# Performance work log

Measured on AMD Instinct MI355X. Metric: run time of the kernel, lower is better.

## Reference

```python
import jax, jax.numpy as jnp
from jax import lax
import numpy as np

Bn, DM, HH, WW = 2, 192, 64, 64   # batch, d_model, H, W (H==W required by transpose-stack)
DI = 384   # d_inner = ssm_ratio * d_model
DS = 16    # ssm_d_state
ND = 4     # n_directions
CG = 12    # c_group
LN_EPS = 1e-5


def setup_inputs() -> dict:
    key = jax.random.key(0)
    k = jax.random.split(key, 16)
    w = lambda i, shape: jax.random.normal(k[i], shape, jnp.float32) * 0.05
    return {
        "x": jax.random.normal(k[0], (Bn, DM, HH, WW), jnp.float32),
        "in_proj_w": w(1, (DI, DM)),
        "dwconv_w": w(2, (DI, 1, 3, 3)),
        "dwconv_b": w(3, (DI,)),
        "x_down_w": w(4, (DS, DI)),
        "w_up_w": w(5, (CG * DI, DS)),
        "l_up_w": w(6, (ND * DI, DS)),
        "u_up_w": w(7, (ND * DI, DS)),
        "d_up_w": w(8, (ND * DI, DS)),
        "m_w": w(9, (ND,)),
        "grn_gamma": w(10, (DI,)),
        "grn_beta": w(11, (DI,)),
        "norm_w": 1.0 + w(12, (DI,)),
        "norm_b": w(13, (DI,)),
        "out_proj_w": w(14, (DM, DI)),
    }


def _conv1x1(w, x):
    return jnp.einsum('oc,bchw->bohw', w, x)


def _gate_recurrent(X, B, G1, G2, G3):
    # H[:, :, h, w] = B*X + G1*H[h-1,w-1] + G2*H[h,w-1] + G3*H[h+1,w-1]
    # sequential over width; vectorized over batch/channel/height via a column scan.
    def step(hprev, col):  # hprev: [B, C, H]
        xw, bw, g1w, g2w, g3w = col
        z = jnp.zeros_like(hprev[:, :, :1])
        up = jnp.concatenate([z, hprev[:, :, :-1]], axis=2)   # H[h-1, w-1]
        dn = jnp.concatenate([hprev[:, :, 1:], z], axis=2)    # H[h+1, w-1]
        h = bw * xw + g1w * up + g2w * hprev + g3w * dn
        return h, h

    cols = tuple(jnp.moveaxis(t, 3, 0) for t in (X, B, G1, G2, G3))  # [W, B, C, H]
    h0 = jnp.zeros(X.shape[:3], X.dtype)
    _, ys = lax.scan(step, h0, cols)
    return jnp.moveaxis(ys, 0, 3)  # [B, C, H, W]


def _normalize_w(Gl, Gm, Gr):
    gl, gm, gr = jax.nn.sigmoid(Gl), jax.nn.sigmoid(Gm), jax.nn.sigmoid(Gr)
    s = gl + gm + gr
    s = s.at[:, :, 0, :].set(gm[:, :, 0, :] + gr[:, :, 0, :])
    s = s.at[:, :, -1, :].set(gl[:, :, -1, :] + gm[:, :, -1, :])
    s = jnp.maximum(s, 1e-7)
    return gl / s, gm / s, gr / s


def reference(x, in_proj_w, dwconv_w, dwconv_b, x_down_w, w_up_w, l_up_w, u_up_w,
              d_up_w, m_w, grn_gamma, grn_beta, norm_w, norm_b, out_proj_w):
    Bsz = x.shape[0]
    # in_proj (1x1, no bias) + SiLU + depthwise 3x3 conv
    h = jax.nn.silu(_conv1x1(in_proj_w, x))
    h = lax.conv_general_dilated(h, dwconv_w, (1, 1), ((1, 1), (1, 1)),
                                 feature_group_count=DI) + dwconv_b[None, :, None, None]
    # forward_corev1
    xp = _conv1x1(x_down_w, h)            # [B, DS, H, W]
    ws = _conv1x1(w_up_w, xp)             # [B, 12*DI, H, W]
    Ls = _conv1x1(l_up_w, xp)             # [B, 4*DI, H, W]
    Us = _conv1x1(u_up_w, xp)
    Ds = _conv1x1(d_up_w, xp)
    hT = jnp.swapaxes(h, 2, 3)            # requires H==W
    xs = jnp.concatenate([h, hT, h[..., ::-1], hT[..., ::-1]], axis=1)  # [B, 4*DI, H, W]
    G1, G2, G3 = jnp.split(ws, 3, axis=1)
    g1, g2, g3 = _normalize_w(G1, G2, G3)
    out = _gate_recurrent(xs, Ls, g1, g2, g3)
    out = out * Us + xs * Ds
    # merge directions: view [B, 4, DI*H, W], 1x1 conv 4->1
    out = out.reshape(Bsz, ND, DI * HH, WW)
    y = jnp.einsum('d,bdxw->bxw', m_w, out).reshape(Bsz, DI, HH, WW)
    # LayerNorm2d over channel dim
    mu = y.mean(axis=1, keepdims=True)
    var = ((y - mu) ** 2).mean(axis=1, keepdims=True)
    y = (y - mu) * lax.rsqrt(var + LN_EPS) * norm_w[None, :, None, None] + norm_b[None, :, None, None]
    # GRN
    Gx = jnp.sqrt(jnp.sum(y * y, axis=(2, 3), keepdims=True))        # [B, C, 1, 1]
    Nx = Gx / (Gx.mean(axis=1, keepdims=True) + 1e-6)
    y = grn_gamma[None, :, None, None] * (y * Nx) + grn_beta[None, :, None, None] + y
    # out_proj (1x1, no bias)
    return _conv1x1(out_proj_w, y)
```

## Files before the change

kernel.cpp:

```cpp
#include <hip/hip_runtime.h>
#include <math.h>

#define Bn 2
#define DM 192
#define DI 384
#define DS 16
#define HH 64
#define WW 64
#define HW 4096
#define ND 4

typedef __attribute__((ext_vector_type(2))) float v2f;
union Q4 { float4 f4; v2f v2[2]; };

__device__ __forceinline__ float fastrcp(float x) { return __builtin_amdgcn_rcpf(x); }
__device__ __forceinline__ float fsig(float x) {
    return fastrcp(1.0f + __expf(-x));
}

#define WLANE(r, s, L) asm("v_writelane_b32 %0, %1, " #L : "+v"(r) : "s"(s))

__device__ __forceinline__ float shift_up(float x) {
    int xi = __float_as_int(x);
    int r = __builtin_amdgcn_mov_dpp(xi, 0x111, 0xF, 0xF, true);
    int t15 = __builtin_amdgcn_readlane(xi, 15);
    int t31 = __builtin_amdgcn_readlane(xi, 31);
    int t47 = __builtin_amdgcn_readlane(xi, 47);
    WLANE(r, t15, 16);
    WLANE(r, t31, 32);
    WLANE(r, t47, 48);
    return __int_as_float(r);
}
__device__ __forceinline__ float shift_dn(float x) {
    int xi = __float_as_int(x);
    int r = __builtin_amdgcn_mov_dpp(xi, 0x101, 0xF, 0xF, true);
    int t16 = __builtin_amdgcn_readlane(xi, 16);
    int t32 = __builtin_amdgcn_readlane(xi, 32);
    int t48 = __builtin_amdgcn_readlane(xi, 48);
    WLANE(r, t16, 15);
    WLANE(r, t32, 31);
    WLANE(r, t48, 47);
    return __int_as_float(r);
}

__global__ __launch_bounds__(256, 3) void k_inproj(const float* __restrict__ x,
                                                   const float* __restrict__ w,
                                                   float* __restrict__ hpre) {
    int og = blockIdx.y, b = blockIdx.z;
    int p = blockIdx.x * 256 + threadIdx.x;
    const float* wr = w + (size_t)og * 16 * DM;
    const float* xb = x + (size_t)b * DM * HW + p;
    float acc[16];
#pragma unroll
    for (int j = 0; j < 16; ++j) acc[j] = 0.f;
    for (int c = 0; c < DM; c += 4) {
        float x0 = xb[(size_t)(c + 0) * HW];
        float x1 = xb[(size_t)(c + 1) * HW];
        float x2 = xb[(size_t)(c + 2) * HW];
        float x3 = xb[(size_t)(c + 3) * HW];
#pragma unroll
        for (int j = 0; j < 16; ++j) {
            const float* wj = wr + j * DM + c;
            acc[j] = fmaf(wj[0], x0, fmaf(wj[1], x1, fmaf(wj[2], x2, fmaf(wj[3], x3, acc[j]))));
        }
    }
    float* hb = hpre + (size_t)b * DI * HW + (size_t)(og * 16) * HW + p;
#pragma unroll
    for (int j = 0; j < 16; ++j) {
        float v = acc[j];
        hb[(size_t)j * HW] = v * fastrcp(1.0f + __expf(-v));
    }
}

__global__ __launch_bounds__(256) void k_dwconv(const float* __restrict__ hpre,
                                                const float* __restrict__ w,
                                                const float* __restrict__ bias,
                                                float* __restrict__ h) {
    int c = blockIdx.y, b = blockIdx.z;
    int p = blockIdx.x * 256 + threadIdx.x;
    int i = p >> 6, j = p & 63;
    const float* wp = w + c * 9;
    const float* src = hpre + ((size_t)b * DI + c) * HW;
    float acc = bias[c];
#pragma unroll
    for (int di = -1; di <= 1; ++di) {
        int ii = i + di;
        if (ii < 0 || ii >= HH) continue;
#pragma unroll
        for (int dj = -1; dj <= 1; ++dj) {
            int jj = j + dj;
            if (jj < 0 || jj >= WW) continue;
            acc = fmaf(wp[(di + 1) * 3 + (dj + 1)], src[ii * WW + jj], acc);
        }
    }
    h[((size_t)b * DI + c) * HW + p] = acc;
}

__global__ __launch_bounds__(256) void k_xdown(const float* __restrict__ h,
                                               const float* __restrict__ w,
                                               float* __restrict__ xpt) {
    __shared__ float red[4][64][17];
    int tid = threadIdx.x;
    int px = tid & 63, cw = tid >> 6;
    int gp = blockIdx.x * 64 + px;
    int b = gp >> 12, p = gp & 4095;
    const float* hb = h + (size_t)b * DI * HW + p;
    int c0 = cw * 96;
    float a[16];
#pragma unroll
    for (int s = 0; s < 16; ++s) a[s] = 0.f;
    for (int cc = 0; cc < 96; cc += 4) {
        float h0 = hb[(size_t)(c0 + cc + 0) * HW];
        float h1 = hb[(size_t)(c0 + cc + 1) * HW];
        float h2 = hb[(size_t)(c0 + cc + 2) * HW];
        float h3 = hb[(size_t)(c0 + cc + 3) * HW];
#pragma unroll
        for (int s = 0; s < 16; ++s) {
            const float* ws = w + (size_t)s * DI + c0 + cc;
            a[s] = fmaf(ws[0], h0, fmaf(ws[1], h1, fmaf(ws[2], h2, fmaf(ws[3], h3, a[s]))));
        }
    }
#pragma unroll
    for (int s = 0; s < 16; ++s) red[cw][px][s] = a[s];
    __syncthreads();
    int sg = tid >> 6;
    float4 r;
    float* o = &r.x;
#pragma unroll
    for (int j = 0; j < 4; ++j) {
        int s = sg * 4 + j;
        o[j] = red[0][px][s] + red[1][px][s] + red[2][px][s] + red[3][px][s];
    }
    int hp = p >> 6, wp_ = p & 63;
    reinterpret_cast<float4*>(xpt)[(size_t)b * (HW * 4) + (wp_ * 4 + sg) * 64 + hp] = r;
}

__device__ __forceinline__ float dot16p(const v2f* __restrict__ W,
                                        const Q4& a0, const Q4& a1,
                                        const Q4& a2, const Q4& a3) {
    v2f t0 = W[0] * a0.v2[0];
    v2f t1 = W[1] * a0.v2[1];
    t0 = __builtin_elementwise_fma(W[2], a1.v2[0], t0);
    t1 = __builtin_elementwise_fma(W[3], a1.v2[1], t1);
    t0 = __builtin_elementwise_fma(W[4], a2.v2[0], t0);
    t1 = __builtin_elementwise_fma(W[5], a2.v2[1], t1);
    t0 = __builtin_elementwise_fma(W[6], a3.v2[0], t0);
    t1 = __builtin_elementwise_fma(W[7], a3.v2[1], t1);
    v2f t = t0 + t1;
    return t.x + t.y;
}

__global__ __launch_bounds__(256, 3) void k_scan(const float* __restrict__ h,
                                                 const float* __restrict__ xpt,
                                                 const float* __restrict__ wup,
                                                 const float* __restrict__ lup,
                                                 const float* __restrict__ uup,
                                                 const float* __restrict__ dup,
                                                 const float* __restrict__ mw,
                                                 float* __restrict__ y) {
    int c = blockIdx.x, b = blockIdx.y;
    int tid = threadIdx.x;
    int d = tid >> 6, hl = tid & 63;

    __shared__ float htile[64][65];
    __shared__ float acc[64][65];

    const float* hb = h + ((size_t)b * DI + c) * HW;
    for (int i = tid; i < HW; i += 256) {
        htile[i >> 6][i & 63] = hb[i];
        acc[i >> 6][i & 63] = 0.f;
    }

    int row = d * DI + c;
    const float* p1 = wup + (size_t)row * DS;
    const float* p2 = wup + (size_t)(4 * DI + row) * DS;
    const float* p3 = wup + (size_t)(8 * DI + row) * DS;
    const float* pL = lup + (size_t)row * DS;
    const float* pU = uup + (size_t)row * DS;
    const float* pD = dup + (size_t)row * DS;
    float md = mw[d];
    v2f w1p[8], w2p[8], w3p[8], wLp[8], wUp[8], wDp[8];
#pragma unroll
    for (int k = 0; k < 8; ++k) {
        w1p[k] = *reinterpret_cast<const v2f*>(p1 + 2 * k);
        w2p[k] = *reinterpret_cast<const v2f*>(p2 + 2 * k);
        w3p[k] = *reinterpret_cast<const v2f*>(p3 + 2 * k);
        wLp[k] = *reinterpret_cast<const v2f*>(pL + 2 * k);
        wUp[k] = md * *reinterpret_cast<const v2f*>(pU + 2 * k);
        wDp[k] = md * *reinterpret_cast<const v2f*>(pD + 2 * k);
    }

    int xstep = (d & 1) ? 65 : 1;
    int xbase = (d & 1) ? hl : hl * 65;
    if (d & 2) { xbase += xstep * 63; xstep = -xstep; }
    const float* xptr = &htile[0][0] + xbase;

    bool isTop = (hl == 0), isBot = (hl == 63);
    float topMul = isTop ? 0.f : 1.f;
    float botMul = isBot ? 0.f : 1.f;

    float* accp = &acc[hl][0];

    const float4* xg = reinterpret_cast<const float4*>(xpt) + (size_t)b * (HW * 4) + hl;

#define LOADQ(R0, R1, R2, R3, wcol) { \
    const float4* pp_ = xg + (size_t)(wcol) * 256; \
    R0.f4 = pp_[0]; R1.f4 = pp_[64]; R2.f4 = pp_[128]; R3.f4 = pp_[192]; }

#define PREP(g1S, g2S, g3S, invS, LS, US, DvS, XS, R0, R1, R2, R3) { \
    g1S = dot16p(w1p, R0, R1, R2, R3); \
    g2S = dot16p(w2p, R0, R1, R2, R3); \
    g3S = dot16p(w3p, R0, R1, R2, R3); \
    LS  = dot16p(wLp, R0, R1, R2, R3); \
    US  = dot16p(wUp, R0, R1, R2, R3); \
    DvS = dot16p(wDp, R0, R1, R2, R3); \
    g1S = fsig(g1S); g2S = fsig(g2S); g3S = fsig(g3S); \
    float ss_ = fmaf(g1S, topMul, fmaf(g3S, botMul, g2S)); \
    invS = fastrcp(fmaxf(ss_, 1e-7f)); \
    XS = *xptr; xptr += xstep; }

#define COMB(g1S, g2S, g3S, invS, LS, US, DvS, XS) { \
    float upv_ = topMul * shift_up(hprev); \
    float dnv_ = botMul * shift_dn(hprev); \
    float hnew_ = fmaf(LS, XS, invS * fmaf(g1S, upv_, fmaf(g2S, hprev, g3S * dnv_))); \
    atomicAdd(accp, fmaf(hnew_, US, XS * DvS)); accp += 1; \
    hprev = hnew_; }

    Q4 A0, A1, A2, A3, B0, B1, B2, B3;
    float g1a, g2a, g3a, inva, La, Ua, Dva, Xa;
    float g1b, g2b, g3b, invb, Lb, Ub, Dvb, Xb;
    float hprev = 0.f;

    LOADQ(A0, A1, A2, A3, 0);
    __syncthreads();
    LOADQ(B0, B1, B2, B3, 1);

    for (int w = 0; w < 64; w += 2) {
        PREP(g1a, g2a, g3a, inva, La, Ua, Dva, Xa, A0, A1, A2, A3);
        int wn2 = (w + 2 < 64) ? w + 2 : 63;
        LOADQ(A0, A1, A2, A3, wn2);
        COMB(g1a, g2a, g3a, inva, La, Ua, Dva, Xa);
        PREP(g1b, g2b, g3b, invb, Lb, Ub, Dvb, Xb, B0, B1, B2, B3);
        int wn3 = (w + 3 < 64) ? w + 3 : 63;
        LOADQ(B0, B1, B2, B3, wn3);
        COMB(g1b, g2b, g3b, invb, Lb, Ub, Dvb, Xb);
    }
#undef LOADQ
#undef PREP
#undef COMB

    __syncthreads();
    float* yb = y + ((size_t)b * DI + c) * HW;
    for (int i = tid; i < HW; i += 256) yb[i] = acc[i >> 6][i & 63];
}

__global__ __launch_bounds__(256) void k_ln(float* __restrict__ y,
                                            const float* __restrict__ nw,
                                            const float* __restrict__ nb) {
    int lpx = threadIdx.x & 15, chunk = threadIdx.x >> 4;
    int gp = blockIdx.x * 16 + lpx;
    int b = gp >> 12, p = gp & 4095;
    float* yb = y + (size_t)b * DI * HW + p;

    float vv[24];
    float s = 0.f, s2 = 0.f;
#pragma unroll
    for (int ci = 0; ci < 24; ++ci) {
        float v = yb[(size_t)(chunk * 24 + ci) * HW];
        vv[ci] = v;
        s += v;
        s2 = fmaf(v, v, s2);
    }
    __shared__ float S[16][17], S2[16][17];
    S[chunk][lpx] = s;
    S2[chunk][lpx] = s2;
    __syncthreads();
    float ts = 0.f, ts2 = 0.f;
#pragma unroll
    for (int k = 0; k < 16; ++k) { ts += S[k][lpx]; ts2 += S2[k][lpx]; }
    float mu = ts * (1.0f / DI);
    float var = ts2 * (1.0f / DI) - mu * mu;
    float inv = rsqrtf(var + 1e-5f);
#pragma unroll
    for (int ci = 0; ci < 24; ++ci) {
        int cch = chunk * 24 + ci;
        float v = (vv[ci] - mu) * inv;
        yb[(size_t)cch * HW] = fmaf(v, nw[cch], nb[cch]);
    }
}

__global__ __launch_bounds__(256) void k_grnsum(const float* __restrict__ y,
                                                float* __restrict__ gx) {
    int c = blockIdx.x, b = blockIdx.y;
    const float* yb = y + ((size_t)b * DI + c) * HW;
    float s = 0.f;
#pragma unroll 4
    for (int i = threadIdx.x; i < HW; i += 256) {
        float v = yb[i];
        s = fmaf(v, v, s);
    }
#pragma unroll
    for (int o = 32; o > 0; o >>= 1) s += __shfl_down(s, o);
    __shared__ float red[4];
    int wid = threadIdx.x >> 6;
    if ((threadIdx.x & 63) == 0) red[wid] = s;
    __syncthreads();
    if (threadIdx.x == 0) gx[b * DI + c] = sqrtf(red[0] + red[1] + red[2] + red[3]);
}

__global__ __launch_bounds__(256) void k_grnscale(const float* __restrict__ gxv,
                                                  const float* __restrict__ gamma,
                                                  float* __restrict__ sc) {
    int b = blockIdx.x;
    const float* g = gxv + b * DI;
    int cidx = threadIdx.x;
    float gx0 = g[cidx];
    float gx1 = (cidx < DI - 256) ? g[cidx + 256] : 0.f;
    float s = gx0 + gx1;
#pragma unroll
    for (int o = 32; o > 0; o >>= 1) s += __shfl_down(s, o);
    __shared__ float red[4];
    __shared__ float meanv;
    int wid = threadIdx.x >> 6;
    if ((threadIdx.x & 63) == 0) red[wid] = s;
    __syncthreads();
    if (threadIdx.x == 0) meanv = (red[0] + red[1] + red[2] + red[3]) * (1.0f / DI);
    __syncthreads();
    float m = meanv + 1e-6f;
    sc[b * DI + cidx] = 1.0f + gamma[cidx] * (gx0 / m);
    if (cidx < DI - 256)
        sc[b * DI + cidx + 256] = 1.0f + gamma[cidx + 256] * (gx1 / m);
}

__global__ __launch_bounds__(256, 3) void k_outproj(const float* __restrict__ y,
                                                    const float* __restrict__ w,
                                                    const float* __restrict__ sc_all,
                                                    const float* __restrict__ beta,
                                                    float* __restrict__ out) {
    int og = blockIdx.y, b = blockIdx.z;
    int p = blockIdx.x * 256 + threadIdx.x;
    const float* wr = w + (size_t)og * 8 * DI;
    const float* scb = sc_all + b * DI;
    const float* yb = y + (size_t)b * DI * HW + p;
    float acc[8];
#pragma unroll
    for (int j = 0; j < 8; ++j) acc[j] = 0.f;
    for (int c = 0; c < DI; c += 4) {
        float v0 = fmaf(yb[(size_t)(c + 0) * HW], scb[c + 0], beta[c + 0]);
        float v1 = fmaf(yb[(size_t)(c + 1) * HW], scb[c + 1], beta[c + 1]);
        float v2 = fmaf(yb[(size_t)(c + 2) * HW], scb[c + 2], beta[c + 2]);
        float v3 = fmaf(yb[(size_t)(c + 3) * HW], scb[c + 3], beta[c + 3]);
#pragma unroll
        for (int j = 0; j < 8; ++j) {
            const float* wj = wr + j * DI + c;
            acc[j] = fmaf(wj[0], v0, fmaf(wj[1], v1, fmaf(wj[2], v2, fmaf(wj[3], v3, acc[j]))));
        }
    }
    float* ob = out + (size_t)b * DM * HW + (size_t)(og * 8) * HW + p;
#pragma unroll
    for (int j = 0; j < 8; ++j) ob[(size_t)j * HW] = acc[j];
}

extern "C" void kernel_launch(void* const* d_in, const int* in_sizes, int n_in,
                              void* d_out, int out_size, void* d_ws, size_t ws_size,
                              hipStream_t stream) {
    (void)in_sizes; (void)n_in; (void)out_size; (void)ws_size;
    const float* x          = (const float*)d_in[0];
    const float* in_proj_w  = (const float*)d_in[1];
    const float* dwconv_w   = (const float*)d_in[2];
    const float* dwconv_b   = (const float*)d_in[3];
    const float* x_down_w   = (const float*)d_in[4];
    const float* w_up_w     = (const float*)d_in[5];
    const float* l_up_w     = (const float*)d_in[6];
    const float* u_up_w     = (const float*)d_in[7];
    const float* d_up_w     = (const float*)d_in[8];
    const float* m_w        = (const float*)d_in[9];
    const float* grn_gamma  = (const float*)d_in[10];
    const float* grn_beta   = (const float*)d_in[11];
    const float* norm_w     = (const float*)d_in[12];
    const float* norm_b     = (const float*)d_in[13];
    const float* out_proj_w = (const float*)d_in[14];

    float* ws = (float*)d_ws;
    const size_t NBIG = (size_t)Bn * DI * HW;
    float* hpre = ws;
    float* hbuf = ws + NBIG;
    float* xpt  = ws + 2 * NBIG;
    float* gx   = ws + 2 * NBIG + (size_t)Bn * HW * DS;
    float* sc   = gx + Bn * DI;
    float* y    = hpre;

    k_inproj<<<dim3(16, 24, 2), 256, 0, stream>>>(x, in_proj_w, hpre);
    k_dwconv<<<dim3(16, DI, Bn), 256, 0, stream>>>(hpre, dwconv_w, dwconv_b, hbuf);
    k_xdown<<<dim3(128), 256, 0, stream>>>(hbuf, x_down_w, xpt);
    k_scan<<<dim3(DI, Bn), 256, 0, stream>>>(hbuf, xpt, w_up_w, l_up_w, u_up_w,
                                             d_up_w, m_w, y);
    k_ln<<<dim3(512), 256, 0, stream>>>(y, norm_w, norm_b);
    k_grnsum<<<dim3(DI, Bn), 256, 0, stream>>>(y, gx);
    k_grnscale<<<dim3(Bn), 256, 0, stream>>>(gx, grn_gamma, sc);
    k_outproj<<<dim3(16, 24, 2), 256, 0, stream>>>(y, out_proj_w, sc, grn_beta,
                                                   (float*)d_out);
}
```

Baseline: 201.9 us.

## Fuse GRN sum-of-squares into LayerNorm and GRN scale into out_proj

The LayerNorm kernel now also accumulates per-channel sums of squares of its output, reducing them in shared memory and adding them to a global buffer with atomics. This removes the separate k_grnsum pass that re-read the whole activation tensor. The GRN scale computation is folded into the prologue of every out_proj block, which removes the k_grnscale launch but recomputes the scale redundantly in each block. It also adds a memset, per-block atomics, and about 25 KB of extra shared memory in k_ln.

```diff
diff --git a/kernel.cpp b/kernel.cpp
--- a/kernel.cpp
+++ b/kernel.cpp
@@ -256,7 +256,8 @@
 
 __global__ __launch_bounds__(256) void k_ln(float* __restrict__ y,
                                             const float* __restrict__ nw,
-                                            const float* __restrict__ nb) {
+                                            const float* __restrict__ nb,
+                                            float* __restrict__ gxsum) {
     int lpx = threadIdx.x & 15, chunk = threadIdx.x >> 4;
     int gp = blockIdx.x * 16 + lpx;
     int b = gp >> 12, p = gp & 4095;
@@ -272,6 +273,7 @@
         s2 = fmaf(v, v, s2);
     }
     __shared__ float S[16][17], S2[16][17];
+    __shared__ float ss[16][385];
     S[chunk][lpx] = s;
     S2[chunk][lpx] = s2;
     __syncthreads();
@@ -285,71 +287,57 @@
     for (int ci = 0; ci < 24; ++ci) {
         int cch = chunk * 24 + ci;
         float v = (vv[ci] - mu) * inv;
-        yb[(size_t)cch * HW] = fmaf(v, nw[cch], nb[cch]);
-    }
-}
-
-__global__ __launch_bounds__(256) void k_grnsum(const float* __restrict__ y,
-                                                float* __restrict__ gx) {
-    int c = blockIdx.x, b = blockIdx.y;
-    const float* yb = y + ((size_t)b * DI + c) * HW;
-    float s = 0.f;
-#pragma unroll 4
-    for (int i = threadIdx.x; i < HW; i += 256) {
-        float v = yb[i];
-        s = fmaf(v, v, s);
-    }
-#pragma unroll
-    for (int o = 32; o > 0; o >>= 1) s += __shfl_down(s, o);
-    __shared__ float red[4];
-    int wid = threadIdx.x >> 6;
-    if ((threadIdx.x & 63) == 0) red[wid] = s;
-    __syncthreads();
-    if (threadIdx.x == 0) gx[b * DI + c] = sqrtf(red[0] + red[1] + red[2] + red[3]);
-}
-
-__global__ __launch_bounds__(256) void k_grnscale(const float* __restrict__ gxv,
-                                                  const float* __restrict__ gamma,
-                                                  float* __restrict__ sc) {
-    int b = blockIdx.x;
-    const float* g = gxv + b * DI;
-    int cidx = threadIdx.x;
-    float gx0 = g[cidx];
-    float gx1 = (cidx < DI - 256) ? g[cidx + 256] : 0.f;
-    float s = gx0 + gx1;
-#pragma unroll
-    for (int o = 32; o > 0; o >>= 1) s += __shfl_down(s, o);
-    __shared__ float red[4];
-    __shared__ float meanv;
-    int wid = threadIdx.x >> 6;
-    if ((threadIdx.x & 63) == 0) red[wid] = s;
-    __syncthreads();
-    if (threadIdx.x == 0) meanv = (red[0] + red[1] + red[2] + red[3]) * (1.0f / DI);
-    __syncthreads();
-    float m = meanv + 1e-6f;
-    sc[b * DI + cidx] = 1.0f + gamma[cidx] * (gx0 / m);
-    if (cidx < DI - 256)
-        sc[b * DI + cidx + 256] = 1.0f + gamma[cidx + 256] * (gx1 / m);
+        float o = fmaf(v, nw[cch], nb[cch]);
+        yb[(size_t)cch * HW] = o;
+        ss[lpx][cch] = o * o;
+    }
+    __syncthreads();
+    for (int cc = threadIdx.x; cc < DI; cc += 256) {
+        float t = 0.f;
+#pragma unroll
+        for (int k = 0; k < 16; ++k) t += ss[k][cc];
+        atomicAdd(&gxsum[b * DI + cc], t);
+    }
 }
 
 __global__ __launch_bounds__(256, 3) void k_outproj(const float* __restrict__ y,
                                                     const float* __restrict__ w,
-                                                    const float* __restrict__ sc_all,
+                                                    const float* __restrict__ gxsum,
+                                                    const float* __restrict__ gamma,
                                                     const float* __restrict__ beta,
                                                     float* __restrict__ out) {
     int og = blockIdx.y, b = blockIdx.z;
-    int p = blockIdx.x * 256 + threadIdx.x;
+    int tid = threadIdx.x;
+    __shared__ float scl[DI];
+    __shared__ float red[4];
+    __shared__ float meanv;
+    {
+        const float* g = gxsum + b * DI;
+        float g0 = sqrtf(g[tid]);
+        float g1 = (tid < DI - 256) ? sqrtf(g[tid + 256]) : 0.f;
+        float sgx = g0 + g1;
+#pragma unroll
+        for (int o = 32; o > 0; o >>= 1) sgx += __shfl_down(sgx, o);
+        if ((tid & 63) == 0) red[tid >> 6] = sgx;
+        __syncthreads();
+        if (tid == 0) meanv = (red[0] + red[1] + red[2] + red[3]) * (1.0f / DI);
+        __syncthreads();
+        float m = meanv + 1e-6f;
+        scl[tid] = 1.0f + gamma[tid] * (g0 / m);
+        if (tid < DI - 256) scl[tid + 256] = 1.0f + gamma[tid + 256] * (g1 / m);
+        __syncthreads();
+    }
+    int p = blockIdx.x * 256 + tid;
     const float* wr = w + (size_t)og * 8 * DI;
-    const float* scb = sc_all + b * DI;
     const float* yb = y + (size_t)b * DI * HW + p;
     float acc[8];
 #pragma unroll
     for (int j = 0; j < 8; ++j) acc[j] = 0.f;
     for (int c = 0; c < DI; c += 4) {
-        float v0 = fmaf(yb[(size_t)(c + 0) * HW], scb[c + 0], beta[c + 0]);
-        float v1 = fmaf(yb[(size_t)(c + 1) * HW], scb[c + 1], beta[c + 1]);
-        float v2 = fmaf(yb[(size_t)(c + 2) * HW], scb[c + 2], beta[c + 2]);
-        float v3 = fmaf(yb[(size_t)(c + 3) * HW], scb[c + 3], beta[c + 3]);
+        float v0 = fmaf(yb[(size_t)(c + 0) * HW], scl[c + 0], beta[c + 0]);
+        float v1 = fmaf(yb[(size_t)(c + 1) * HW], scl[c + 1], beta[c + 1]);
+        float v2 = fmaf(yb[(size_t)(c + 2) * HW], scl[c + 2], beta[c + 2]);
+        float v3 = fmaf(yb[(size_t)(c + 3) * HW], scl[c + 3], beta[c + 3]);
 #pragma unroll
         for (int j = 0; j < 8; ++j) {
             const float* wj = wr + j * DI + c;
@@ -387,7 +375,6 @@
     float* hbuf = ws + NBIG;
     float* xpt  = ws + 2 * NBIG;
     float* gx   = ws + 2 * NBIG + (size_t)Bn * HW * DS;
-    float* sc   = gx + Bn * DI;
     float* y    = hpre;
 
     k_inproj<<<dim3(16, 24, 2), 256, 0, stream>>>(x, in_proj_w, hpre);
@@ -395,9 +382,8 @@
     k_xdown<<<dim3(128), 256, 0, stream>>>(hbuf, x_down_w, xpt);
     k_scan<<<dim3(DI, Bn), 256, 0, stream>>>(hbuf, xpt, w_up_w, l_up_w, u_up_w,
                                              d_up_w, m_w, y);
-    k_ln<<<dim3(512), 256, 0, stream>>>(y, norm_w, norm_b);
-    k_grnsum<<<dim3(DI, Bn), 256, 0, stream>>>(y, gx);
-    k_grnscale<<<dim3(Bn), 256, 0, stream>>>(gx, grn_gamma, sc);
-    k_outproj<<<dim3(16, 24, 2), 256, 0, stream>>>(y, out_proj_w, sc, grn_beta,
-                                                   (float*)d_out);
-}
+    hipMemsetAsync(gx, 0, Bn * DI * sizeof(float), stream);
+    k_ln<<<dim3(512), 256, 0, stream>>>(y, norm_w, norm_b, gx);
+    k_outproj<<<dim3(16, 24, 2), 256, 0, stream>>>(y, out_proj_w, gx, grn_gamma,
+                                                   grn_beta, (float*)d_out);
+}
```

Result: no change. 202.0 us (median of 2 runs) (+0.1%).
